# Performance work log

Measured on AMD Instinct MI355X. Metric: run time of the kernel, lower is better.

## Reference

```python
import jax, jax.numpy as jnp
import numpy as np

# --- CQT configuration derived from the layer's __init__ defaults ---
SR = 44100
N_OCTAVES = 7
BINS_PER_SEMITONE = 3
BPO = BINS_PER_SEMITONE * 12            # 36 bins per octave
N_BINS = BPO * N_OCTAVES                # 252 bins
HOP = (int(SR * 11 / 1000.0) // 4) * 4  # 485 -> 484 (hop - hop % 4)
FMIN = 32.70319566257483                # librosa default fmin = C1
Q = 1.0 / (2.0 ** (1.0 / BPO) - 1.0)    # constant-Q factor, filter_scale=1

_FREQS = FMIN * 2.0 ** (np.arange(N_BINS) / BPO)   # [252] center freqs
_LENGTHS = Q * SR / _FREQS                         # per-bin window lengths
MAX_LEN = int(np.ceil(_LENGTHS[0]))                # longest kernel (lowest bin)
CENTER = MAX_LEN // 2
SIG_LEN = 220500                                   # 5 s of audio
N_FRAMES = 1 + SIG_LEN // HOP                      # 456 (centered framing)


def _cqt_kernels():
    """Complex CQT kernel bank, returned as (real, imag) of shape [N_BINS, MAX_LEN].
    Each bin uses a Hann window of its own constant-Q length, centered in MAX_LEN,
    modulated at its center frequency; L1-normalized window and 1/sqrt(L) scaling
    (matching librosa's norm=1 filters with scale=True)."""
    t = jnp.arange(MAX_LEN, dtype=jnp.float32) - CENTER          # centered time axis
    freqs = jnp.asarray(_FREQS, dtype=jnp.float32)[:, None]      # [252, 1]
    L = jnp.asarray(_LENGTHS, dtype=jnp.float32)[:, None]        # [252, 1]
    two_pi = 2.0 * np.pi
    # Hann window of length L_i centered at t=0, zero outside |t| < L_i/2
    win = jnp.where(jnp.abs(t)[None, :] < L / 2,
                    0.5 * (1.0 + jnp.cos(two_pi * t[None, :] / L)),
                    0.0)
    ang = two_pi * freqs * t[None, :] / SR
    norm = win.sum(axis=-1, keepdims=True) * jnp.sqrt(L)
    kr = win * jnp.cos(ang) / norm
    ki = win * jnp.sin(ang) / norm
    return kr, ki


def setup_inputs() -> dict:
    key = jax.random.key(0)
    signal = jax.random.normal(key, (SIG_LEN,), dtype=jnp.float32)
    return {"signal": signal}


def reference(signal) -> jnp.ndarray:
    kr, ki = _cqt_kernels()                                      # [252, MAX_LEN] each
    padded = jnp.pad(signal, (CENTER, CENTER))                   # center=True framing
    idx = (jnp.arange(N_FRAMES)[:, None] * HOP
           + jnp.arange(MAX_LEN)[None, :])                       # [456, MAX_LEN]
    frames = padded[idx]                                         # [456, MAX_LEN]
    cr = frames @ kr.T                                           # [456, 252] real part
    ci = frames @ ki.T                                           # [456, 252] imag part
    mag = jnp.sqrt(cr * cr + ci * ci)                            # |CQT|
    return mag.T                                                 # [252, 456] = (n_bins, n_frames)
```

## Files before the change

kernel.cpp:

```cpp
#include <hip/hip_runtime.h>
#include <hip/hip_bf16.h>
#include <math.h>

#define NBINS    252
#define NFRAMES  456
#define HOPSZ    484
#define SIGLEN   220500
#define PADOFF   34688
#define XBF_ELEMS 317440
#define SRD      44100.0
#define FMIND    32.70319566257483
#define MAXCH    264
#define SC       32

typedef unsigned short ushort_t;
typedef __attribute__((ext_vector_type(8))) short bf16x8;
typedef __attribute__((ext_vector_type(4))) float f32x4;

struct ChunkTab { int2 e[MAXCH]; };
struct GTab     { int2 e[16]; };

__device__ __forceinline__ ushort_t f2bf(float x) {
  __hip_bfloat16 h = __float2bfloat16(x);
  return *reinterpret_cast<ushort_t*>(&h);
}

__global__ __launch_bounds__(256) void pad_bf16(const float* __restrict__ sig,
                                                ushort_t* __restrict__ xbf) {
  int i = blockIdx.x * 256 + threadIdx.x;
  if (i < XBF_ELEMS) {
    int s = i - PADOFF;
    float v = (s >= 0 && s < SIGLEN) ? sig[s] : 0.0f;
    xbf[i] = f2bf(v);
  }
}

__global__ void prep_kernel(float4* __restrict__ binc, float* __restrict__ nrm) {
  int b = threadIdx.x;
  if (b >= 256) return;
  if (b < NBINS) {
    const double PI = 3.14159265358979323846;
    double freq = FMIND * exp2((double)b / 36.0);
    double fos = freq / SRD;
    double Q = 1.0 / (exp2(1.0 / 36.0) - 1.0);
    double L = Q * SRD / freq;
    int T = (int)(L * 0.5);
    double N = (double)(2 * T + 1);
    double win_sum = 0.5 * N - 0.5 * (sin(PI * (N - L) / L) / sin(PI / L));
    binc[b] = make_float4((float)fos, (float)(1.0 / L), (float)T, 0.0f);
    nrm[b] = (float)(1.0 / (win_sum * sqrt(L)));
  } else {
    binc[b] = make_float4(0.0f, 0.0f, -1.0f, 0.0f);
  }
}

__global__ __launch_bounds__(512) void cqt_fused(const ushort_t* __restrict__ xbf,
                                                 const float4* __restrict__ binc,
                                                 float2* __restrict__ partial,
                                                 ChunkTab tab) {
  __shared__ ushort_t blds[SC * 1024];

  const int tid  = threadIdx.x;
  const int lane = tid & 63;
  const int bl   = lane & 15, kb = lane >> 4;
  const int c    = blockIdx.y;
  const int st   = blockIdx.x;
  const int g    = tab.e[c].x, jadj = tab.e[c].y;

  {
    const float4 bc = binc[g * 16 + bl];
    const float fos = bc.x, invL = bc.y, Tf = bc.z;
    const int ksub = tid >> 6;
#pragma unroll
    for (int kq = 0; kq < 4; ++kq) {
      const int ks = ksub + kq * 8;
      const int t0 = jadj + ks * 32 + kb * 8;
      union { ushort_t u[8]; uint4 v; } pr, pi;
#pragma unroll
      for (int j = 0; j < 8; ++j) {
        const float tt = (float)(t0 + j);
        float kr = 0.0f, ki = 0.0f;
        if (fabsf(tt) <= Tf) {
          float w = 0.5f + 0.5f * __cosf(6.2831853f * (tt * invL));
          float r = fos * tt; r -= rintf(r);
          float s, cc; __sincosf(6.2831853f * r, &s, &cc);
          kr = w * cc; ki = w * s;
        }
        pr.u[j] = f2bf(kr); pi.u[j] = f2bf(ki);
      }
      *reinterpret_cast<uint4*>(&blds[ks * 1024 + lane * 8])       = pr.v;
      *reinterpret_cast<uint4*>(&blds[ks * 1024 + 512 + lane * 8]) = pi.v;
    }
  }
  __syncthreads();

  const int w = tid >> 6;
  const int fbase = st * 256 + w * 32;
  const ushort_t* pA0 = xbf + PADOFF + (fbase + bl) * HOPSZ + jadj + kb * 8;
  const ushort_t* pA1 = pA0 + 16 * HOPSZ;

  f32x4 ar0 = {0.f, 0.f, 0.f, 0.f};
  f32x4 ai0 = ar0, ar1 = ar0, ai1 = ar0;

#pragma unroll 8
  for (int ks = 0; ks < SC; ++ks) {
    union { uint2 q[2]; bf16x8 v; } a0, a1;
    a0.q[0] = *reinterpret_cast<const uint2*>(pA0 + ks * 32);
    a0.q[1] = *reinterpret_cast<const uint2*>(pA0 + ks * 32 + 4);
    a1.q[0] = *reinterpret_cast<const uint2*>(pA1 + ks * 32);
    a1.q[1] = *reinterpret_cast<const uint2*>(pA1 + ks * 32 + 4);
    union { uint4 q; bf16x8 v; } bk, bi;
    bk.q = *reinterpret_cast<const uint4*>(&blds[ks * 1024 + lane * 8]);
    bi.q = *reinterpret_cast<const uint4*>(&blds[ks * 1024 + 512 + lane * 8]);
    ar0 = __builtin_amdgcn_mfma_f32_16x16x32_bf16(a0.v, bk.v, ar0, 0, 0, 0);
    ai0 = __builtin_amdgcn_mfma_f32_16x16x32_bf16(a0.v, bi.v, ai0, 0, 0, 0);
    ar1 = __builtin_amdgcn_mfma_f32_16x16x32_bf16(a1.v, bk.v, ar1, 0, 0, 0);
    ai1 = __builtin_amdgcn_mfma_f32_16x16x32_bf16(a1.v, bi.v, ai1, 0, 0, 0);
  }

  float2* pp = partial + ((size_t)(c * 2 + st) * 256 + w * 32) * 16 + bl;
  const int row = kb * 4;
#pragma unroll
  for (int r = 0; r < 4; ++r) {
    pp[(size_t)(row + r) * 16]      = make_float2(ar0[r], ai0[r]);
    pp[(size_t)(row + r + 16) * 16] = make_float2(ar1[r], ai1[r]);
  }
}

__global__ __launch_bounds__(256) void fin_kernel(const float2* __restrict__ partial,
                                                  const float* __restrict__ nrm,
                                                  float* __restrict__ out, GTab gt) {
  int id = blockIdx.x * 256 + threadIdx.x;
  if (id >= NBINS * NFRAMES) return;
  int b = id / NFRAMES;
  int f = id - b * NFRAMES;
  int g = b >> 4, bl = b & 15;
  int st = f >> 8, fl = f & 255;
  int c0 = gt.e[g].x, nc = gt.e[g].y;
  float cr = 0.f, ci = 0.f;
  for (int c = c0; c < c0 + nc; ++c) {
    float2 v = partial[((size_t)(c * 2 + st) * 256 + fl) * 16 + bl];
    cr += v.x; ci += v.y;
  }
  out[id] = nrm[b] * sqrtf(cr * cr + ci * ci);
}

extern "C" void kernel_launch(void* const* d_in, const int* in_sizes, int n_in,
                              void* d_out, int out_size, void* d_ws, size_t ws_size,
                              hipStream_t stream) {
  const float* sig = (const float*)d_in[0];
  float* out = (float*)d_out;
  char* ws = (char*)d_ws;

  ChunkTab ctab; GTab gtab;
  int nch = 0;
  const double Q = 1.0 / (exp2(1.0 / 36.0) - 1.0);
  for (int gq = 0; gq < 16; ++gq) {
    double freq = FMIND * exp2((double)(16 * gq) / 36.0);
    double L = Q * SRD / freq;
    int T = (int)(L * 0.5);
    int r = (4 - (T & 3)) & 3;
    int tstart = -(T + r);
    int ntaps = 2 * T + 1 + r;
    int chunks = (ntaps + SC * 32 - 1) / (SC * 32);
    gtab.e[gq].x = nch; gtab.e[gq].y = chunks;
    for (int k = 0; k < chunks; ++k) {
      ctab.e[nch].x = gq; ctab.e[nch].y = tstart + k * SC * 32; ++nch;
    }
  }
  for (int i = nch; i < MAXCH; ++i) { ctab.e[i].x = 0; ctab.e[i].y = 0; }

  ushort_t* xbf = (ushort_t*)ws;
  size_t off = (size_t)XBF_ELEMS * 2;
  float4* binc = (float4*)(ws + off);  off += 256 * sizeof(float4);
  float* nrm   = (float*)(ws + off);   off += 256 * sizeof(float);
  float2* partial = (float2*)(ws + ((off + 255) & ~(size_t)255));

  pad_bf16<<<(XBF_ELEMS + 255) / 256, 256, 0, stream>>>(sig, xbf);
  prep_kernel<<<1, 256, 0, stream>>>(binc, nrm);
  cqt_fused<<<dim3(2, nch), 512, 0, stream>>>(xbf, binc, partial, ctab);
  fin_kernel<<<(NBINS * NFRAMES + 255) / 256, 256, 0, stream>>>(partial, nrm, out, gtab);
}
```

Before: 121.5 us.

## Pre-tile framed signal into MFMA fragment layout and fold prep into host constants

Replaces the padded bf16 signal buffer with a pre-transposed, frame-tiled bf16 array so each MFMA A-fragment is a single contiguous 16-byte load instead of two strided 8-byte loads. Bin parameters and normalization now come from host-computed kernel arguments, which removes the prep kernel launch. The finalize kernel is reorganized to read partials as float4 per group. The tiled buffer duplicates overlapping frame samples, so it is much larger and costs more global writes in the transpose step, in exchange for coalesced reads in the main GEMM.

```diff
diff --git a/kernel.cpp b/kernel.cpp
--- a/kernel.cpp
+++ b/kernel.cpp
@@ -6,8 +6,10 @@
 #define NFRAMES  456
 #define HOPSZ    484
 #define SIGLEN   220500
-#define PADOFF   34688
-#define XBF_ELEMS 317440
+#define TSTART0  (-34688)
+#define KMAX     69632
+#define KB8      8704
+#define NFT      32
 #define SRD      44100.0
 #define FMIND    32.70319566257483
 #define MAXCH    264
@@ -18,63 +20,79 @@
 typedef __attribute__((ext_vector_type(4))) float f32x4;
 
 struct ChunkTab { int2 e[MAXCH]; };
-struct GTab     { int2 e[16]; };
+struct GroupC {
+  float fosg[16];
+  float invLg[16];
+  float ratio[16];
+  ushort_t Tfu[256];
+};
+struct FinC { float nrm[256]; int2 gt[16]; };
 
 __device__ __forceinline__ ushort_t f2bf(float x) {
   __hip_bfloat16 h = __float2bfloat16(x);
   return *reinterpret_cast<ushort_t*>(&h);
 }
 
-__global__ __launch_bounds__(256) void pad_bf16(const float* __restrict__ sig,
-                                                ushort_t* __restrict__ xbf) {
-  int i = blockIdx.x * 256 + threadIdx.x;
-  if (i < XBF_ELEMS) {
-    int s = i - PADOFF;
-    float v = (s >= 0 && s < SIGLEN) ? sig[s] : 0.0f;
-    xbf[i] = f2bf(v);
-  }
-}
-
-__global__ void prep_kernel(float4* __restrict__ binc, float* __restrict__ nrm) {
-  int b = threadIdx.x;
-  if (b >= 256) return;
-  if (b < NBINS) {
-    const double PI = 3.14159265358979323846;
-    double freq = FMIND * exp2((double)b / 36.0);
-    double fos = freq / SRD;
-    double Q = 1.0 / (exp2(1.0 / 36.0) - 1.0);
-    double L = Q * SRD / freq;
-    int T = (int)(L * 0.5);
-    double N = (double)(2 * T + 1);
-    double win_sum = 0.5 * N - 0.5 * (sin(PI * (N - L) / L) / sin(PI / L));
-    binc[b] = make_float4((float)fos, (float)(1.0 / L), (float)T, 0.0f);
-    nrm[b] = (float)(1.0 / (win_sum * sqrt(L)));
-  } else {
-    binc[b] = make_float4(0.0f, 0.0f, -1.0f, 0.0f);
-  }
-}
-
-__global__ __launch_bounds__(512) void cqt_fused(const ushort_t* __restrict__ xbf,
-                                                 const float4* __restrict__ binc,
+__global__ __launch_bounds__(256) void transpose_kernel(const float* __restrict__ sig,
+                                                        ushort_t* __restrict__ At) {
+  __shared__ ushort_t lds[16][1032];
+  const int kbg = blockIdx.x;
+  const int ft  = blockIdx.y;
+  const int t   = threadIdx.x;
+
+  {
+    const int r = t & 15, c16 = t >> 4;
+    const int sbase = (ft * 16 + r) * HOPSZ + TSTART0 + kbg * 1024 + c16 * 64;
+#pragma unroll
+    for (int cc = 0; cc < 16; ++cc) {
+      const int s = sbase + cc * 4;
+      ushort_t o0, o1, o2, o3;
+      if (s >= 0 && s + 3 < SIGLEN) {
+        const float4 v = *reinterpret_cast<const float4*>(sig + s);
+        o0 = f2bf(v.x); o1 = f2bf(v.y); o2 = f2bf(v.z); o3 = f2bf(v.w);
+      } else {
+        o0 = (s + 0 >= 0 && s + 0 < SIGLEN) ? f2bf(sig[s + 0]) : (ushort_t)0;
+        o1 = (s + 1 >= 0 && s + 1 < SIGLEN) ? f2bf(sig[s + 1]) : (ushort_t)0;
+        o2 = (s + 2 >= 0 && s + 2 < SIGLEN) ? f2bf(sig[s + 2]) : (ushort_t)0;
+        o3 = (s + 3 >= 0 && s + 3 < SIGLEN) ? f2bf(sig[s + 3]) : (ushort_t)0;
+      }
+      const int col = c16 * 64 + cc * 4;
+      lds[r][col + 0] = o0; lds[r][col + 1] = o1;
+      lds[r][col + 2] = o2; lds[r][col + 3] = o3;
+    }
+  }
+  __syncthreads();
+
+  const size_t OB = ((size_t)ft * KB8 + (size_t)kbg * 128) * 128;
+  const int fr = t & 15;
+#pragma unroll
+  for (int q = 0; q < 8; ++q) {
+    const int kb = q * 16 + (t >> 4);
+    const uint4 v = *reinterpret_cast<const uint4*>(&lds[fr][kb * 8]);
+    *reinterpret_cast<uint4*>(At + OB + ((size_t)kb * 16 + fr) * 8) = v;
+  }
+}
+
+__global__ __launch_bounds__(512) void cqt_fused(const ushort_t* __restrict__ At,
                                                  float2* __restrict__ partial,
-                                                 ChunkTab tab) {
+                                                 ChunkTab tab, GroupC gc) {
   __shared__ ushort_t blds[SC * 1024];
-
   const int tid  = threadIdx.x;
   const int lane = tid & 63;
   const int bl   = lane & 15, kb = lane >> 4;
   const int c    = blockIdx.y;
   const int st   = blockIdx.x;
-  const int g    = tab.e[c].x, jadj = tab.e[c].y;
+  const int g    = tab.e[c].x, jrel = tab.e[c].y;
 
   {
-    const float4 bc = binc[g * 16 + bl];
-    const float fos = bc.x, invL = bc.y, Tf = bc.z;
+    const float fos  = gc.fosg[g]  * gc.ratio[bl];
+    const float invL = gc.invLg[g] * gc.ratio[bl];
+    const float Tf   = (float)gc.Tfu[g * 16 + bl];
     const int ksub = tid >> 6;
 #pragma unroll
     for (int kq = 0; kq < 4; ++kq) {
       const int ks = ksub + kq * 8;
-      const int t0 = jadj + ks * 32 + kb * 8;
+      const int t0 = TSTART0 + jrel + ks * 32 + kb * 8;
       union { ushort_t u[8]; uint4 v; } pr, pi;
 #pragma unroll
       for (int j = 0; j < 8; ++j) {
@@ -83,8 +101,8 @@
         if (fabsf(tt) <= Tf) {
           float w = 0.5f + 0.5f * __cosf(6.2831853f * (tt * invL));
           float r = fos * tt; r -= rintf(r);
-          float s, cc; __sincosf(6.2831853f * r, &s, &cc);
-          kr = w * cc; ki = w * s;
+          float s, cc2; __sincosf(6.2831853f * r, &s, &cc2);
+          kr = w * cc2; ki = w * s;
         }
         pr.u[j] = f2bf(kr); pi.u[j] = f2bf(ki);
       }
@@ -96,20 +114,18 @@
 
   const int w = tid >> 6;
   const int fbase = st * 256 + w * 32;
-  const ushort_t* pA0 = xbf + PADOFF + (fbase + bl) * HOPSZ + jadj + kb * 8;
-  const ushort_t* pA1 = pA0 + 16 * HOPSZ;
+  const int ft0 = fbase >> 4;
+  const ushort_t* pA0 = At + (((size_t)ft0 * KB8 + (jrel >> 3) + kb) * 16 + bl) * 8;
+  const ushort_t* pA1 = pA0 + (size_t)KB8 * 128;
 
   f32x4 ar0 = {0.f, 0.f, 0.f, 0.f};
   f32x4 ai0 = ar0, ar1 = ar0, ai1 = ar0;
 
 #pragma unroll 8
   for (int ks = 0; ks < SC; ++ks) {
-    union { uint2 q[2]; bf16x8 v; } a0, a1;
-    a0.q[0] = *reinterpret_cast<const uint2*>(pA0 + ks * 32);
-    a0.q[1] = *reinterpret_cast<const uint2*>(pA0 + ks * 32 + 4);
-    a1.q[0] = *reinterpret_cast<const uint2*>(pA1 + ks * 32);
-    a1.q[1] = *reinterpret_cast<const uint2*>(pA1 + ks * 32 + 4);
-    union { uint4 q; bf16x8 v; } bk, bi;
+    union { uint4 q; bf16x8 v; } a0, a1, bk, bi;
+    a0.q = *reinterpret_cast<const uint4*>(pA0 + (size_t)ks * 512);
+    a1.q = *reinterpret_cast<const uint4*>(pA1 + (size_t)ks * 512);
     bk.q = *reinterpret_cast<const uint4*>(&blds[ks * 1024 + lane * 8]);
     bi.q = *reinterpret_cast<const uint4*>(&blds[ks * 1024 + 512 + lane * 8]);
     ar0 = __builtin_amdgcn_mfma_f32_16x16x32_bf16(a0.v, bk.v, ar0, 0, 0, 0);
@@ -128,21 +144,29 @@
 }
 
 __global__ __launch_bounds__(256) void fin_kernel(const float2* __restrict__ partial,
-                                                  const float* __restrict__ nrm,
-                                                  float* __restrict__ out, GTab gt) {
-  int id = blockIdx.x * 256 + threadIdx.x;
-  if (id >= NBINS * NFRAMES) return;
-  int b = id / NFRAMES;
-  int f = id - b * NFRAMES;
-  int g = b >> 4, bl = b & 15;
-  int st = f >> 8, fl = f & 255;
-  int c0 = gt.e[g].x, nc = gt.e[g].y;
-  float cr = 0.f, ci = 0.f;
+                                                  float* __restrict__ out, FinC fc) {
+  const int g  = blockIdx.x;
+  const int st = blockIdx.y;
+  const int fq = blockIdx.z;
+  const int t  = threadIdx.x;
+  const int c0 = fc.gt[g].x, nc = fc.gt[g].y;
+
+  float cr[4] = {0.f, 0.f, 0.f, 0.f}, ci[4] = {0.f, 0.f, 0.f, 0.f};
   for (int c = c0; c < c0 + nc; ++c) {
-    float2 v = partial[((size_t)(c * 2 + st) * 256 + fl) * 16 + bl];
-    cr += v.x; ci += v.y;
-  }
-  out[id] = nrm[b] * sqrtf(cr * cr + ci * ci);
+    const float4* b4 = reinterpret_cast<const float4*>(
+        partial + (size_t)(c * 2 + st) * 4096 + fq * 1024 + t * 4);
+    const float4 v0 = b4[0], v1 = b4[1];
+    cr[0] += v0.x; ci[0] += v0.y; cr[1] += v0.z; ci[1] += v0.w;
+    cr[2] += v1.x; ci[2] += v1.y; cr[3] += v1.z; ci[3] += v1.w;
+  }
+#pragma unroll
+  for (int i = 0; i < 4; ++i) {
+    const int flat = fq * 1024 + t * 4 + i;
+    const int fl = flat >> 4, bl = flat & 15;
+    const int f = st * 256 + fl, b = g * 16 + bl;
+    if (f < NFRAMES && b < NBINS)
+      out[(size_t)b * NFRAMES + f] = fc.nrm[b] * sqrtf(cr[i] * cr[i] + ci[i] * ci[i]);
+  }
 }
 
 extern "C" void kernel_launch(void* const* d_in, const int* in_sizes, int n_in,
@@ -152,32 +176,47 @@
   float* out = (float*)d_out;
   char* ws = (char*)d_ws;
 
-  ChunkTab ctab; GTab gtab;
+  ChunkTab ctab; GroupC gc; FinC fc;
+  const double PI = 3.14159265358979323846;
+  const double Q = 1.0 / (exp2(1.0 / 36.0) - 1.0);
   int nch = 0;
-  const double Q = 1.0 / (exp2(1.0 / 36.0) - 1.0);
-  for (int gq = 0; gq < 16; ++gq) {
-    double freq = FMIND * exp2((double)(16 * gq) / 36.0);
+  for (int g = 0; g < 16; ++g) {
+    double freq = FMIND * exp2((double)(16 * g) / 36.0);
     double L = Q * SRD / freq;
     int T = (int)(L * 0.5);
-    int r = (4 - (T & 3)) & 3;
+    int r = (8 - (T & 7)) & 7;
     int tstart = -(T + r);
     int ntaps = 2 * T + 1 + r;
-    int chunks = (ntaps + SC * 32 - 1) / (SC * 32);
-    gtab.e[gq].x = nch; gtab.e[gq].y = chunks;
+    int chunks = (ntaps + 1023) / 1024;
+    gc.fosg[g] = (float)(freq / SRD);
+    gc.invLg[g] = (float)(1.0 / L);
+    fc.gt[g].x = nch; fc.gt[g].y = chunks;
+    int jrel0 = tstart - TSTART0;
     for (int k = 0; k < chunks; ++k) {
-      ctab.e[nch].x = gq; ctab.e[nch].y = tstart + k * SC * 32; ++nch;
+      ctab.e[nch].x = g; ctab.e[nch].y = jrel0 + k * 1024; ++nch;
     }
   }
   for (int i = nch; i < MAXCH; ++i) { ctab.e[i].x = 0; ctab.e[i].y = 0; }
-
-  ushort_t* xbf = (ushort_t*)ws;
-  size_t off = (size_t)XBF_ELEMS * 2;
-  float4* binc = (float4*)(ws + off);  off += 256 * sizeof(float4);
-  float* nrm   = (float*)(ws + off);   off += 256 * sizeof(float);
-  float2* partial = (float2*)(ws + ((off + 255) & ~(size_t)255));
-
-  pad_bf16<<<(XBF_ELEMS + 255) / 256, 256, 0, stream>>>(sig, xbf);
-  prep_kernel<<<1, 256, 0, stream>>>(binc, nrm);
-  cqt_fused<<<dim3(2, nch), 512, 0, stream>>>(xbf, binc, partial, ctab);
-  fin_kernel<<<(NBINS * NFRAMES + 255) / 256, 256, 0, stream>>>(partial, nrm, out, gtab);
-}
+  for (int bl = 0; bl < 16; ++bl) gc.ratio[bl] = (float)exp2((double)bl / 36.0);
+  for (int b = 0; b < 256; ++b) {
+    if (b < NBINS) {
+      double freq = FMIND * exp2((double)b / 36.0);
+      double L = Q * SRD / freq;
+      int T = (int)(L * 0.5);
+      double N = (double)(2 * T + 1);
+      double win_sum = 0.5 * N - 0.5 * (sin(PI * (N - L) / L) / sin(PI / L));
+      gc.Tfu[b] = (ushort_t)T;
+      fc.nrm[b] = (float)(1.0 / (win_sum * sqrt(L)));
+    } else {
+      gc.Tfu[b] = 0; fc.nrm[b] = 0.0f;
+    }
+  }
+
+  ushort_t* At = (ushort_t*)ws;
+  size_t off = (size_t)NFT * KB8 * 128 * sizeof(ushort_t);
+  float2* partial = (float2*)(ws + off);
+
+  transpose_kernel<<<dim3(68, NFT), 256, 0, stream>>>(sig, At);
+  cqt_fused<<<dim3(2, nch), 512, 0, stream>>>(At, partial, ctab, gc);
+  fin_kernel<<<dim3(16, 2, 4), 256, 0, stream>>>(partial, out, fc);
+}
```

Measured after the change: 161.4 us. +32.9%, slower.
